# Performance work log

Hardware: AMD Instinct MI355X
Metric: run time of the kernel (lower is better)

The kernel has to match this reference:

```python
import jax, jax.numpy as jnp
from jax import lax
import numpy as np

CH = 16
STAGES = 6
DN = ('NDHWC', 'DHWIO', 'NDHWC')


def setup_inputs() -> dict:
    key = jax.random.key(0)
    ks = jax.random.split(key, 16)
    B, G = 8, 64
    x = jax.random.normal(ks[0], (B, G, G, G, 1), dtype=jnp.float32)
    mask = jax.random.randint(ks[1], (B, G, G, G), 0, 2, dtype=jnp.int32)
    meta = jax.random.normal(ks[2], (B, 3), dtype=jnp.float32)
    sched = jax.random.normal(ks[3], (B, 128), dtype=jnp.float32)
    s = 0.05
    w_stem = jax.random.normal(ks[4], (5, 5, 5, 1, CH), dtype=jnp.float32) * s
    w_stages = jax.random.normal(ks[5], (STAGES, 3, 3, 3, CH, CH), dtype=jnp.float32) * s
    meta_w1 = jax.random.normal(ks[6], (3, 32), dtype=jnp.float32) * s
    meta_b1 = jnp.zeros((32,), jnp.float32)
    meta_w2 = jax.random.normal(ks[7], (32, 16), dtype=jnp.float32) * s
    meta_b2 = jnp.zeros((16,), jnp.float32)
    mat_w = jax.random.normal(ks[8], (CH * STAGES + 16, 128), dtype=jnp.float32) * s
    mat_b = jnp.zeros((128,), jnp.float32)
    sch_w = jax.random.normal(ks[9], (128, 128), dtype=jnp.float32) * s
    sch_b = jnp.zeros((128,), jnp.float32)
    f1_w = jax.random.normal(ks[10], (256, 128), dtype=jnp.float32) * s
    f1_b = jnp.zeros((128,), jnp.float32)
    f2_w = jax.random.normal(ks[11], (128, 1), dtype=jnp.float32) * s
    f2_b = jnp.zeros((1,), jnp.float32)
    return dict(x=x, mask=mask, meta=meta, sched=sched, w_stem=w_stem,
                w_stages=w_stages, meta_w1=meta_w1, meta_b1=meta_b1,
                meta_w2=meta_w2, meta_b2=meta_b2, mat_w=mat_w, mat_b=mat_b,
                sch_w=sch_w, sch_b=sch_b, f1_w=f1_w, f1_b=f1_b,
                f2_w=f2_w, f2_b=f2_b)


def _pool_mask(m):
    # ME stride-2 output coords = unique(coords // 2): 2x2x2 max-pool, ceil sizes
    return lax.reduce_window(m, jnp.float32(0), lax.max,
                             (1, 2, 2, 2), (1, 2, 2, 2), 'SAME')


def reference(x, mask, meta, sched, w_stem, w_stages, meta_w1, meta_b1,
              meta_w2, meta_b2, mat_w, mat_b, sch_w, sch_b,
              f1_w, f1_b, f2_w, f2_b):
    m = mask.astype(x.dtype)
    feats = x * m[..., None]                       # zero features off-mask
    y = lax.conv_general_dilated(feats, w_stem, (1, 1, 1), 'SAME',
                                 dimension_numbers=DN)
    y = jnp.maximum(y * m[..., None], 0.0)         # stem: conv + mask + ReLU
    pools = []
    for i in range(STAGES):
        y = lax.conv_general_dilated(y, w_stages[i], (2, 2, 2),
                                     [(1, 1), (1, 1), (1, 1)],
                                     dimension_numbers=DN)
        m = _pool_mask(m)
        y = jnp.maximum(y * m[..., None], 0.0)
        denom = jnp.maximum(m.sum(axis=(1, 2, 3)), 1.0)   # occupied voxels
        pools.append(y.sum(axis=(1, 2, 3)) / denom[:, None])
    pools = jnp.concatenate(pools, axis=1)                 # [B, CH*STAGES]
    h = jax.nn.relu(meta[:, :3] @ meta_w1 + meta_b1)
    meta_emb = h @ meta_w2 + meta_b2                        # [B,16]
    m_emb = jax.nn.relu(jnp.concatenate([pools, meta_emb], 1) @ mat_w + mat_b)
    s_emb = jax.nn.relu(sched @ sch_w + sch_b)
    z = jnp.concatenate([m_emb, s_emb], axis=1)             # [B,256]
    z = jax.nn.relu(z @ f1_w + f1_b)
    return z @ f2_w + f2_b                                  # [B,1]
```

## Files before the change

### kernel.cpp

```cpp
#include <hip/hip_runtime.h>

#define CH 16
#define NB 8

typedef unsigned short u16;
typedef unsigned int u32;
typedef __attribute__((ext_vector_type(8))) short s16x8;
typedef __attribute__((ext_vector_type(4))) float f32x4;

__device__ __forceinline__ float bflo(u32 u) { return __uint_as_float(u << 16); }
__device__ __forceinline__ float bfhi(u32 u) { return __uint_as_float(u & 0xffff0000u); }
__device__ __forceinline__ u32 bfrnd(float f) {
  u32 u = __float_as_uint(f);
  return (u + 0x7fffu + ((u >> 16) & 1u)) >> 16;
}
__device__ __forceinline__ u32 packbf(float lo, float hi) {
  return bfrnd(lo) | (bfrnd(hi) << 16);
}

__global__ __launch_bounds__(256) void bprep_kernel(
    const float* __restrict__ w_stg, u16* __restrict__ bpre)
{
  const int e = blockIdx.x * 256 + (int)threadIdx.x;
  if (e >= 3 * 7168) return;
  const int s = e / 7168, r0 = e % 7168;
  const int i = r0 >> 9;
  const int r = r0 & 511;
  const int l = r >> 3, j = r & 7;
  const int tap = 2 * i + (l >> 5);
  const int cin = ((l >> 4) & 1) * 8 + j;
  const int n = l & 15;
  const float* w = w_stg + s * 27 * 256;
  const float val = (tap < 27) ? w[(tap * 16 + cin) * 16 + n] : 0.f;
  bpre[s * 7168 + i * 512 + l * 8 + j] = (u16)bfrnd(val);
}

__global__ __launch_bounds__(256) void stem_mfma(
    const float* __restrict__ x, const int* __restrict__ mask,
    const float* __restrict__ wst, u16* __restrict__ yout,
    float* __restrict__ pool_sum, float* __restrict__ cnt)
{
  __shared__ u16 tl[144 * 24];
  __shared__ u16 cp[8 * 1168];

  const int b = blockIdx.y;
  const int u = blockIdx.x;
  const int tb = ((u & 7) << 6) | (u >> 3);
  const int z0 = (tb >> 6) * 8;
  const int y0 = ((tb >> 3) & 7) * 8;
  const int x0 = (tb & 7) * 8;
  const int tid = threadIdx.x;

  if (tb == 0) {
    if (tid < 96) pool_sum[b * 96 + tid] = 0.f;
    else if (tid < 102) cnt[b * 6 + (tid - 96)] = 0.f;
  }

  const int lane = tid & 63;
  const int wv = tid >> 6;
  const int n = lane & 15;
  const int quad = lane >> 4;
  const int vy = n >> 2, vx = n & 3;

  s16x8 wf[7];
#pragma unroll
  for (int i = 0; i < 7; ++i) {
    const int r = i * 4 + quad;
#pragma unroll
    for (int j = 0; j < 8; ++j) {
      float v = 0.f;
      if (r < 25 && j < 5) v = wst[(r * 5 + j) * 16 + n];
      wf[i][j] = (short)bfrnd(v);
    }
  }

  for (int i = tid; i < 1728; i += 256) {
    const int row = i / 12;
    const int lx = i - row * 12;
    const int lz = row / 12;
    const int ly = row - lz * 12;
    const int gz = z0 + lz - 2, gy = y0 + ly - 2, gx = x0 + lx - 2;
    float v = 0.f;
    if ((unsigned)gz < 64u && (unsigned)gy < 64u && (unsigned)gx < 64u) {
      const int gi = ((b * 64 + gz) * 64 + gy) * 64 + gx;
      v = x[gi] * (float)mask[gi];
    }
    tl[row * 24 + lx] = (u16)bfrnd(v);
  }
  __syncthreads();

  if (tid < 144) {
    const uint4 a = *(const uint4*)&tl[tid * 24];
    const uint2 bq = *(const uint2*)&tl[tid * 24 + 8];
    u32 c[7];
    c[0] = a.x; c[1] = a.y; c[2] = a.z; c[3] = a.w;
    c[4] = bq.x; c[5] = bq.y; c[6] = 0u;
    u32 d[7];
#pragma unroll
    for (int k = 0; k < 6; ++k) d[k] = (c[k] >> 16) | (c[k + 1] << 16);
    d[6] = c[6] >> 16;
    uint4* dst = (uint4*)&cp[tid * 8];
    dst[0 * 146] = make_uint4(c[0], c[1], c[2], c[3]);
    dst[1 * 146] = make_uint4(d[0], d[1], d[2], d[3]);
    dst[2 * 146] = make_uint4(c[1], c[2], c[3], c[4]);
    dst[3 * 146] = make_uint4(d[1], d[2], d[3], d[4]);
    dst[4 * 146] = make_uint4(c[2], c[3], c[4], c[5]);
    dst[5 * 146] = make_uint4(d[2], d[3], d[4], d[5]);
    dst[6 * 146] = make_uint4(c[3], c[4], c[5], c[6]);
    dst[7 * 146] = make_uint4(d[3], d[4], d[5], d[6]);
  }
  __syncthreads();

  int doff[7];
#pragma unroll
  for (int i = 0; i < 7; ++i) {
    const int r = i * 4 + quad;
    doff[i] = (r < 25) ? ((r / 5) * 12 + (r % 5)) * 8 : 0;
  }

  for (int s = 0; s < 8; ++s) {
    const int sz = (s >> 2) * 4, sy = ((s >> 1) & 1) * 4, sx = (s & 1) * 4;
    const int base =
        (sx + vx) * 1168 + (((sz + wv) * 12) + (sy + vy)) * 8;
    f32x4 acc = {0.f, 0.f, 0.f, 0.f};
#pragma unroll
    for (int i = 0; i < 7; ++i) {
      const s16x8 bf = *(const s16x8*)&cp[base + doff[i]];
      acc = __builtin_amdgcn_mfma_f32_16x16x32_bf16(wf[i], bf, acc, 0, 0, 0);
    }
    const int Z = z0 + sz + wv, Y = y0 + sy + vy, X = x0 + sx + vx;
    const int gi = ((b * 64 + Z) * 64 + Y) * 64 + X;
    const float mv = (float)mask[gi];
    const float f0 = fmaxf(acc[0], 0.f) * mv;
    const float f1 = fmaxf(acc[1], 0.f) * mv;
    const float f2 = fmaxf(acc[2], 0.f) * mv;
    const float f3 = fmaxf(acc[3], 0.f) * mv;
    uint2* op = (uint2*)(yout + (size_t)gi * CH + quad * 4);
    op[0] = make_uint2(packbf(f0, f1), packbf(f2, f3));
  }
}

__global__ __launch_bounds__(256) void stage_mfma4(
    const u16* __restrict__ yin, const u16* __restrict__ bpre,
    const int* __restrict__ m_in_i, const float* __restrict__ m_in_f,
    u16* __restrict__ yout, float* __restrict__ m_out,
    float* __restrict__ pool_sum, float* __restrict__ cnt,
    const int S, const int stage)
{
  __shared__ u16 lb[14 * 512];
  __shared__ float lC[4 * 16 * 17];
  __shared__ float lmp[256];

  const int So = S >> 1;
  const int nvox = So * So * So;
  const int b = blockIdx.y;
  const int tid = threadIdx.x;
  const int vg0 = blockIdx.x * 256;

  {
    const uint4* src = (const uint4*)bpre;
    uint4* dst = (uint4*)lb;
    for (int e = tid; e < 896; e += 256) dst[e] = src[e];
  }

  {
    const int vox = vg0 + tid;
    const int oz = vox / (So * So);
    const int oy = (vox / So) % So;
    const int ox = vox % So;
    float mp = 0.f;
#pragma unroll
    for (int dz = 0; dz < 2; ++dz)
#pragma unroll
      for (int dy = 0; dy < 2; ++dy)
#pragma unroll
        for (int dx = 0; dx < 2; ++dx) {
          const int mi =
              ((b * S + 2 * oz + dz) * S + 2 * oy + dy) * S + 2 * ox + dx;
          const float mv = m_in_i ? (float)m_in_i[mi] : m_in_f[mi];
          mp = fmaxf(mp, mv);
        }
    lmp[tid] = mp;
  }
  __syncthreads();

  const int wv = tid >> 6;
  const int lane = tid & 63;
  const int m = lane & 15;
  const int quad = lane >> 4;
  const int qh = quad >> 1;
  const int qlo = quad & 1;

  int izb[4], iyb[4], ixb[4];
#pragma unroll
  for (int g = 0; g < 4; ++g) {
    const int vox = vg0 + wv * 64 + g * 16 + m;
    const int oz = vox / (So * So);
    const int oy = (vox / So) % So;
    const int ox = vox % So;
    izb[g] = 2 * oz - 1;
    iyb[g] = 2 * oy - 1;
    ixb[g] = 2 * ox - 1;
  }

  const s16x8* lbv = (const s16x8*)lb;
  f32x4 acc[4];
#pragma unroll
  for (int g = 0; g < 4; ++g) acc[g] = (f32x4){0.f, 0.f, 0.f, 0.f};

#pragma unroll
  for (int i = 0; i < 14; ++i) {
    const int t0 = 2 * i, t1 = 2 * i + 1;
    const int dz0 = t0 / 9, dy0 = (t0 / 3) % 3, dx0 = t0 % 3;
    const int dz1 = (t1 < 27) ? t1 / 9 : 1;
    const int dy1 = (t1 < 27) ? (t1 / 3) % 3 : 1;
    const int dx1 = (t1 < 27) ? t1 % 3 : 1;
    const int dzq = qh ? dz1 : dz0;
    const int dyq = qh ? dy1 : dy0;
    const int dxq = qh ? dx1 : dx0;

    uint4 ar[4];
#pragma unroll
    for (int g = 0; g < 4; ++g) {
      const int iz = izb[g] + dzq;
      const int iy = iyb[g] + dyq;
      const int ix = ixb[g] + dxq;
      const bool valid = (unsigned)iz < (unsigned)S &&
                         (unsigned)iy < (unsigned)S &&
                         (unsigned)ix < (unsigned)S;
      const int izc = min(max(iz, 0), S - 1);
      const int iyc = min(max(iy, 0), S - 1);
      const int ixc = min(max(ix, 0), S - 1);
      const size_t addr =
          (size_t)(((b * S + izc) * S + iyc) * S + ixc) * 16 + qlo * 8;
      uint4 v = *(const uint4*)(yin + addr);
      v.x = valid ? v.x : 0u;
      v.y = valid ? v.y : 0u;
      v.z = valid ? v.z : 0u;
      v.w = valid ? v.w : 0u;
      ar[g] = v;
    }
    const s16x8 bfrag = lbv[i * 64 + lane];
#pragma unroll
    for (int g = 0; g < 4; ++g)
      acc[g] = __builtin_amdgcn_mfma_f32_16x16x32_bf16(
          __builtin_bit_cast(s16x8, ar[g]), bfrag, acc[g], 0, 0, 0);
  }

  float psum = 0.f;
#pragma unroll
  for (int g = 0; g < 4; ++g) {
    __syncthreads();
    {
      float* lCw = lC + wv * 272;
      const int n = lane & 15;
#pragma unroll
      for (int reg = 0; reg < 4; ++reg) {
        const int row = quad * 4 + reg;
        lCw[row * 17 + n] =
            fmaxf(acc[g][reg], 0.f) * lmp[wv * 64 + g * 16 + row];
      }
    }
    __syncthreads();
    {
      const int vox_l = tid >> 2;
      const int cg = (tid & 3) * 4;
      const float* src = lC + (vox_l >> 4) * 272 + (vox_l & 15) * 17 + cg;
      const float f0 = src[0], f1 = src[1], f2 = src[2], f3 = src[3];
      const int lv = (vox_l >> 4) * 64 + g * 16 + (vox_l & 15);
      const size_t gi = (size_t)b * nvox + vg0 + lv;
      uint2* op = (uint2*)(yout + gi * 16 + cg);
      op[0] = make_uint2(packbf(f0, f1), packbf(f2, f3));
      if ((tid & 3) == 0) m_out[gi] = lmp[lv];
    }
    if (tid < 16) {
      float s = 0.f;
#pragma unroll 16
      for (int v = 0; v < 64; ++v)
        s += lC[(v >> 4) * 272 + (v & 15) * 17 + tid];
      psum += s;
    }
  }
  if (tid < 16) {
    atomicAdd(&pool_sum[(b * 6 + stage) * 16 + tid], psum);
  } else if (tid == 16) {
    float c = 0.f;
#pragma unroll 16
    for (int v = 0; v < 256; ++v) c += lmp[v];
    atomicAdd(&cnt[b * 6 + stage], c);
  }
}

__global__ __launch_bounds__(256) void tail_kernel(
    const u16* __restrict__ y3g, const float* __restrict__ m3g,
    const float* __restrict__ wstg,
    const float* __restrict__ meta, const float* __restrict__ sched,
    const float* __restrict__ mw1, const float* __restrict__ mb1,
    const float* __restrict__ mw2, const float* __restrict__ mb2,
    const float* __restrict__ matw, const float* __restrict__ matb,
    const float* __restrict__ schw, const float* __restrict__ schb,
    const float* __restrict__ f1w, const float* __restrict__ f1b,
    const float* __restrict__ f2w, const float* __restrict__ f2b,
    const float* __restrict__ pool_sum, const float* __restrict__ cnt,
    float* __restrict__ out)
{
  const int b = blockIdx.x;
  const int t = threadIdx.x;
  __shared__ float ly3[8 * 8 * 8 * 16];
  __shared__ float lm3[512];
  __shared__ float ly4[4 * 4 * 4 * 16];
  __shared__ float lm4[64];
  __shared__ float ly5[8 * 16];
  __shared__ float lm5[8];
  __shared__ float lsum[3][16];
  __shared__ float lcnt[3];
  __shared__ float invec[112];
  __shared__ float hbuf[32];
  __shared__ float zbuf[256];
  __shared__ float part[2];

  const uint4* yb = (const uint4*)(y3g + (size_t)b * 8192);
  for (int i = t; i < 1024; i += 256) {
    const uint4 p = yb[i];
    float* d = &ly3[i * 8];
    d[0] = bflo(p.x); d[1] = bfhi(p.x);
    d[2] = bflo(p.y); d[3] = bfhi(p.y);
    d[4] = bflo(p.z); d[5] = bfhi(p.z);
    d[6] = bflo(p.w); d[7] = bfhi(p.w);
  }
  for (int i = t; i < 512; i += 256) lm3[i] = m3g[b * 512 + i];
  __syncthreads();

  {
    const float* w = wstg + 3 * 27 * 256;
    const int vox = t >> 2, cog = (t & 3) * 4;
    const int oz = vox >> 4, oy = (vox >> 2) & 3, ox = vox & 3;
    float acc[4] = {0.f, 0.f, 0.f, 0.f};
#pragma unroll
    for (int dz = 0; dz < 3; ++dz)
#pragma unroll
      for (int dy = 0; dy < 3; ++dy)
#pragma unroll
        for (int dx = 0; dx < 3; ++dx) {
          const int iz = 2 * oz + dz - 1, iy = 2 * oy + dy - 1,
                    ix = 2 * ox + dx - 1;
          const float s = ((unsigned)iz < 8u && (unsigned)iy < 8u &&
                           (unsigned)ix < 8u) ? 1.f : 0.f;
          const int idx = ((min(max(iz, 0), 7) * 8 + min(max(iy, 0), 7)) * 8 +
                           min(max(ix, 0), 7)) * 16;
          const float* wp = w + ((dz * 3 + dy) * 3 + dx) * 256;
#pragma unroll
          for (int ci = 0; ci < 16; ++ci) {
            const float v = ly3[idx + ci] * s;
#pragma unroll
            for (int c = 0; c < 4; ++c)
              acc[c] = fmaf(v, wp[ci * 16 + cog + c], acc[c]);
          }
        }
    float mp = 0.f;
#pragma unroll
    for (int dz = 0; dz < 2; ++dz)
#pragma unroll
      for (int dy = 0; dy < 2; ++dy)
#pragma unroll
        for (int dx = 0; dx < 2; ++dx)
          mp = fmaxf(mp, lm3[((2 * oz + dz) * 8 + 2 * oy + dy) * 8 +
                             2 * ox + dx]);
#pragma unroll
    for (int c = 0; c < 4; ++c)
      ly4[vox * 16 + cog + c] = fmaxf(acc[c], 0.f) * mp;
    if (cog == 0) lm4[vox] = mp;
  }
  __syncthreads();

  if (t < 16) {
    float s = 0.f;
#pragma unroll 16
    for (int v = 0; v < 64; ++v) s += ly4[v * 16 + t];
    lsum[0][t] = s;
  } else if (t == 16) {
    float s = 0.f;
#pragma unroll 16
    for (int v = 0; v < 64; ++v) s += lm4[v];
    lcnt[0] = s;
  }
  float s4val = 0.f, s4mp = 0.f;
  const int vox4 = (t >> 4) & 7, co4 = t & 15;
  if (t < 128) {
    const float* w = wstg + 4 * 27 * 256;
    const int oz = vox4 >> 2, oy = (vox4 >> 1) & 1, ox = vox4 & 1;
    float acc = 0.f;
#pragma unroll
    for (int dz = 0; dz < 3; ++dz)
#pragma unroll
      for (int dy = 0; dy < 3; ++dy)
#pragma unroll
        for (int dx = 0; dx < 3; ++dx) {
          const int iz = 2 * oz + dz - 1, iy = 2 * oy + dy - 1,
                    ix = 2 * ox + dx - 1;
          const float s = ((unsigned)iz < 4u && (unsigned)iy < 4u &&
                           (unsigned)ix < 4u) ? 1.f : 0.f;
          const int idx = ((min(max(iz, 0), 3) * 4 + min(max(iy, 0), 3)) * 4 +
                           min(max(ix, 0), 3)) * 16;
          const float* wp = w + ((dz * 3 + dy) * 3 + dx) * 256 + co4;
#pragma unroll
          for (int ci = 0; ci < 16; ++ci)
            acc = fmaf(ly4[idx + ci] * s, wp[ci * 16], acc);
        }
    float mp = 0.f;
#pragma unroll
    for (int dz = 0; dz < 2; ++dz)
#pragma unroll
      for (int dy = 0; dy < 2; ++dy)
#pragma unroll
        for (int dx = 0; dx < 2; ++dx)
          mp = fmaxf(mp, lm4[((2 * (vox4 >> 2) + dz) * 4 +
                              2 * ((vox4 >> 1) & 1) + dy) * 4 +
                             2 * (vox4 & 1) + dx]);
    s4val = fmaxf(acc, 0.f) * mp;
    s4mp = mp;
  }
  __syncthreads();
  if (t < 128) {
    ly5[vox4 * 16 + co4] = s4val;
    if (co4 == 0) lm5[vox4] = s4mp;
  }
  __syncthreads();

  if (t < 16) {
    float s = 0.f;
#pragma unroll
    for (int v = 0; v < 8; ++v) s += ly5[v * 16 + t];
    lsum[1][t] = s;
  } else if (t == 16) {
    lcnt[1] = lm5[0] + lm5[1] + lm5[2] + lm5[3] + lm5[4] + lm5[5] + lm5[6] +
              lm5[7];
  }
  if (t >= 64 && t < 80) {
    const int co = t - 64;
    const float* w = wstg + 5 * 27 * 256;
    float acc = 0.f;
#pragma unroll
    for (int dz = 0; dz < 3; ++dz)
#pragma unroll
      for (int dy = 0; dy < 3; ++dy)
#pragma unroll
        for (int dx = 0; dx < 3; ++dx) {
          const int iz = dz - 1, iy = dy - 1, ix = dx - 1;
          const float s = ((unsigned)iz < 2u && (unsigned)iy < 2u &&
                           (unsigned)ix < 2u) ? 1.f : 0.f;
          const int idx = ((min(max(iz, 0), 1) * 2 + min(max(iy, 0), 1)) * 2 +
                           min(max(ix, 0), 1)) * 16;
          const float* wp = w + ((dz * 3 + dy) * 3 + dx) * 256 + co;
#pragma unroll
          for (int ci = 0; ci < 16; ++ci)
            acc = fmaf(ly5[idx + ci] * s, wp[ci * 16], acc);
        }
    float mp = 0.f;
#pragma unroll
    for (int v = 0; v < 8; ++v) mp = fmaxf(mp, lm5[v]);
    lsum[2][co] = fmaxf(acc, 0.f) * mp;
    if (co == 0) lcnt[2] = mp;
  }
  __syncthreads();

  if (t < 48) {
    const int s = t >> 4;
    invec[t] = pool_sum[b * 96 + t] / fmaxf(cnt[b * 6 + s], 1.f);
  } else if (t < 96) {
    const int s = (t >> 4) - 3;
    invec[t] = lsum[s][t & 15] / fmaxf(lcnt[s], 1.f);
  } else if (t < 128) {
    const int j = t - 96;
    float h = mb1[j];
#pragma unroll
    for (int k = 0; k < 3; ++k) h = fmaf(meta[b * 3 + k], mw1[k * 32 + j], h);
    hbuf[j] = fmaxf(h, 0.f);
  }
  __syncthreads();
  if (t < 16) {
    float e = mb2[t];
#pragma unroll
    for (int j = 0; j < 32; ++j) e = fmaf(hbuf[j], mw2[j * 16 + t], e);
    invec[96 + t] = e;
  }
  __syncthreads();
  if (t < 128) {
    float a = matb[t];
#pragma unroll 16
    for (int k = 0; k < 112; ++k) a = fmaf(invec[k], matw[k * 128 + t], a);
    zbuf[t] = fmaxf(a, 0.f);
    float s = schb[t];
#pragma unroll 16
    for (int k = 0; k < 128; ++k)
      s = fmaf(sched[b * 128 + k], schw[k * 128 + t], s);
    zbuf[128 + t] = fmaxf(s, 0.f);
  }
  __syncthreads();
  if (t < 128) {
    float a = f1b[t];
#pragma unroll 16
    for (int k = 0; k < 256; ++k) a = fmaf(zbuf[k], f1w[k * 128 + t], a);
    float v = fmaxf(a, 0.f) * f2w[t];
#pragma unroll
    for (int off = 32; off > 0; off >>= 1) v += __shfl_xor(v, off, 64);
    if ((t & 63) == 0) part[t >> 6] = v;
  }
  __syncthreads();
  if (t == 0) out[b] = part[0] + part[1] + f2b[0];
}

extern "C" void kernel_launch(void* const* d_in, const int* in_sizes, int n_in,
                              void* d_out, int out_size, void* d_ws,
                              size_t ws_size, hipStream_t stream)
{
  (void)in_sizes; (void)n_in; (void)out_size; (void)ws_size;
  const float* x      = (const float*)d_in[0];
  const int*   mask   = (const int*)  d_in[1];
  const float* meta   = (const float*)d_in[2];
  const float* sched  = (const float*)d_in[3];
  const float* w_stem = (const float*)d_in[4];
  const float* w_stg  = (const float*)d_in[5];
  const float* mw1    = (const float*)d_in[6];
  const float* mb1    = (const float*)d_in[7];
  const float* mw2    = (const float*)d_in[8];
  const float* mb2    = (const float*)d_in[9];
  const float* matw   = (const float*)d_in[10];
  const float* matb   = (const float*)d_in[11];
  const float* schw   = (const float*)d_in[12];
  const float* schb   = (const float*)d_in[13];
  const float* f1w    = (const float*)d_in[14];
  const float* f1b    = (const float*)d_in[15];
  const float* f2w    = (const float*)d_in[16];
  const float* f2b    = (const float*)d_in[17];
  float* out = (float*)d_out;

  char* ws = (char*)d_ws;
  size_t off = 0;
  auto alloc = [&](size_t nbytes) -> void* {
    void* p = ws + off;
    off += (nbytes + 255) & ~(size_t)255;
    return p;
  };

  u16* y0 = (u16*)alloc((size_t)NB * 64 * 64 * 64 * CH * 2);
  u16* y1 = (u16*)alloc((size_t)NB * 32 * 32 * 32 * CH * 2);
  u16* y2 = (u16*)alloc((size_t)NB * 16 * 16 * 16 * CH * 2);
  u16* y3 = (u16*)alloc((size_t)NB * 8 * 8 * 8 * CH * 2);
  float* m1 = (float*)alloc((size_t)NB * 32 * 32 * 32 * 4);
  float* m2 = (float*)alloc((size_t)NB * 16 * 16 * 16 * 4);
  float* m3 = (float*)alloc((size_t)NB * 8 * 8 * 8 * 4);
  float* pool_sum = (float*)alloc((NB * 96 + NB * 6) * 4);
  float* cnt = pool_sum + NB * 96;
  u16* bpre = (u16*)alloc(3 * 7168 * 2);

  bprep_kernel<<<84, 256, 0, stream>>>(w_stg, bpre);

  stem_mfma<<<dim3(512, NB), 256, 0, stream>>>(x, mask, w_stem, y0,
                                               pool_sum, cnt);

  stage_mfma4<<<dim3(128, NB), 256, 0, stream>>>(
      y0, bpre + 0 * 7168, mask, (const float*)nullptr, y1, m1,
      pool_sum, cnt, 64, 0);
  stage_mfma4<<<dim3(16, NB), 256, 0, stream>>>(
      y1, bpre + 1 * 7168, (const int*)nullptr, m1, y2, m2,
      pool_sum, cnt, 32, 1);
  stage_mfma4<<<dim3(2, NB), 256, 0, stream>>>(
      y2, bpre + 2 * 7168, (const int*)nullptr, m2, y3, m3,
      pool_sum, cnt, 16, 2);

  tail_kernel<<<NB, 256, 0, stream>>>(y3, m3, w_stg, meta, sched,
                                      mw1, mb1, mw2, mb2, matw, matb,
                                      schw, schb, f1w, f1b, f2w, f2b,
                                      pool_sum, cnt, out);
}
```

Baseline: 227.3 us.

## Use MFMA for tail stage-3 conv and split tail work across all threads

The tail kernel's stage-3 conv now runs on bf16 MFMA. It uses a fourth slab of prepacked weights produced by the extended bprep kernel, and each wave reduces a share of the taps before a shared-memory partial-sum reduction. The stage 4/5 convs and the f1 and schedule layers are split across more threads, with the partial sums combined afterwards. The meta MLP is moved earlier to overlap with other work. The intent is to shorten the serial tail, which runs on only 8 blocks. In exchange it adds extra syncs and shared memory, and the stage-3 conv now runs in bf16.

```diff
diff --git a/kernel.cpp b/kernel.cpp
--- a/kernel.cpp
+++ b/kernel.cpp
@@ -22,7 +22,7 @@
     const float* __restrict__ w_stg, u16* __restrict__ bpre)
 {
   const int e = blockIdx.x * 256 + (int)threadIdx.x;
-  if (e >= 3 * 7168) return;
+  if (e >= 4 * 7168) return;
   const int s = e / 7168, r0 = e % 7168;
   const int i = r0 >> 9;
   const int r = r0 & 511;
@@ -293,6 +293,7 @@
 
 __global__ __launch_bounds__(256) void tail_kernel(
     const u16* __restrict__ y3g, const float* __restrict__ m3g,
+    const u16* __restrict__ bpre,
     const float* __restrict__ wstg,
     const float* __restrict__ meta, const float* __restrict__ sched,
     const float* __restrict__ mw1, const float* __restrict__ mb1,
@@ -306,57 +307,99 @@
 {
   const int b = blockIdx.x;
   const int t = threadIdx.x;
-  __shared__ float ly3[8 * 8 * 8 * 16];
+  __shared__ u16 ty3[8192];
   __shared__ float lm3[512];
-  __shared__ float ly4[4 * 4 * 4 * 16];
+  __shared__ float pb[4 * 64 * 17];
+  __shared__ float ly4[64 * 16];
   __shared__ float lm4[64];
+  __shared__ float ps4[256];
   __shared__ float ly5[8 * 16];
   __shared__ float lm5[8];
+  __shared__ float ps5[128];
   __shared__ float lsum[3][16];
   __shared__ float lcnt[3];
   __shared__ float invec[112];
   __shared__ float hbuf[32];
   __shared__ float zbuf[256];
+  __shared__ float psf[256];
   __shared__ float part[2];
 
-  const uint4* yb = (const uint4*)(y3g + (size_t)b * 8192);
-  for (int i = t; i < 1024; i += 256) {
-    const uint4 p = yb[i];
-    float* d = &ly3[i * 8];
-    d[0] = bflo(p.x); d[1] = bfhi(p.x);
-    d[2] = bflo(p.y); d[3] = bfhi(p.y);
-    d[4] = bflo(p.z); d[5] = bfhi(p.z);
-    d[6] = bflo(p.w); d[7] = bfhi(p.w);
-  }
-  for (int i = t; i < 512; i += 256) lm3[i] = m3g[b * 512 + i];
-  __syncthreads();
-
   {
-    const float* w = wstg + 3 * 27 * 256;
-    const int vox = t >> 2, cog = (t & 3) * 4;
+    const uint4* yb = (const uint4*)(y3g + (size_t)b * 8192);
+    uint4* dst = (uint4*)ty3;
+    for (int i = t; i < 1024; i += 256) dst[i] = yb[i];
+    for (int i = t; i < 512; i += 256) lm3[i] = m3g[b * 512 + i];
+  }
+  __syncthreads();
+
+  {
+    const int lane = t & 63;
+    const int wv = t >> 6;
+    const int mm = lane & 15;
+    const int quad = lane >> 4;
+    const int qh = quad >> 1, qlo = quad & 1;
+
+    int iz0[4], iy0[4], ix0[4];
+#pragma unroll
+    for (int g = 0; g < 4; ++g) {
+      const int vox = g * 16 + mm;
+      iz0[g] = 2 * (vox >> 4) - 1;
+      iy0[g] = 2 * ((vox >> 2) & 3) - 1;
+      ix0[g] = 2 * (vox & 3) - 1;
+    }
+    f32x4 a3[4];
+#pragma unroll
+    for (int g = 0; g < 4; ++g) a3[g] = (f32x4){0.f, 0.f, 0.f, 0.f};
+    const s16x8* bp3 = (const s16x8*)(bpre + 3 * 7168);
+#pragma unroll
+    for (int ii = 0; ii < 4; ++ii) {
+      const int i = wv * 4 + ii;
+      if (i < 14) {
+        const int t0 = 2 * i, t1 = 2 * i + 1;
+        const int dz0 = t0 / 9, dy0 = (t0 / 3) % 3, dx0 = t0 % 3;
+        const int dz1 = (t1 < 27) ? t1 / 9 : 1;
+        const int dy1 = (t1 < 27) ? (t1 / 3) % 3 : 1;
+        const int dx1 = (t1 < 27) ? t1 % 3 : 1;
+        const int dzq = qh ? dz1 : dz0;
+        const int dyq = qh ? dy1 : dy0;
+        const int dxq = qh ? dx1 : dx0;
+        uint4 ar[4];
+#pragma unroll
+        for (int g = 0; g < 4; ++g) {
+          const int iz = iz0[g] + dzq;
+          const int iy = iy0[g] + dyq;
+          const int ix = ix0[g] + dxq;
+          const bool valid = (unsigned)iz < 8u && (unsigned)iy < 8u &&
+                             (unsigned)ix < 8u;
+          const int izc = min(max(iz, 0), 7);
+          const int iyc = min(max(iy, 0), 7);
+          const int ixc = min(max(ix, 0), 7);
+          const int ad = ((izc * 8 + iyc) * 8 + ixc) * 16 + qlo * 8;
+          uint4 v = *(const uint4*)&ty3[ad];
+          v.x = valid ? v.x : 0u;
+          v.y = valid ? v.y : 0u;
+          v.z = valid ? v.z : 0u;
+          v.w = valid ? v.w : 0u;
+          ar[g] = v;
+        }
+        const s16x8 bf = bp3[i * 64 + lane];
+#pragma unroll
+        for (int g = 0; g < 4; ++g)
+          a3[g] = __builtin_amdgcn_mfma_f32_16x16x32_bf16(
+              __builtin_bit_cast(s16x8, ar[g]), bf, a3[g], 0, 0, 0);
+      }
+    }
+#pragma unroll
+    for (int g = 0; g < 4; ++g)
+#pragma unroll
+      for (int reg = 0; reg < 4; ++reg)
+        pb[wv * 1088 + (g * 16 + quad * 4 + reg) * 17 + mm] = a3[g][reg];
+  }
+  __syncthreads();
+
+  {
+    const int vox = t >> 2, cg = (t & 3) * 4;
     const int oz = vox >> 4, oy = (vox >> 2) & 3, ox = vox & 3;
-    float acc[4] = {0.f, 0.f, 0.f, 0.f};
-#pragma unroll
-    for (int dz = 0; dz < 3; ++dz)
-#pragma unroll
-      for (int dy = 0; dy < 3; ++dy)
-#pragma unroll
-        for (int dx = 0; dx < 3; ++dx) {
-          const int iz = 2 * oz + dz - 1, iy = 2 * oy + dy - 1,
-                    ix = 2 * ox + dx - 1;
-          const float s = ((unsigned)iz < 8u && (unsigned)iy < 8u &&
-                           (unsigned)ix < 8u) ? 1.f : 0.f;
-          const int idx = ((min(max(iz, 0), 7) * 8 + min(max(iy, 0), 7)) * 8 +
-                           min(max(ix, 0), 7)) * 16;
-          const float* wp = w + ((dz * 3 + dy) * 3 + dx) * 256;
-#pragma unroll
-          for (int ci = 0; ci < 16; ++ci) {
-            const float v = ly3[idx + ci] * s;
-#pragma unroll
-            for (int c = 0; c < 4; ++c)
-              acc[c] = fmaf(v, wp[ci * 16 + cog + c], acc[c]);
-          }
-        }
     float mp = 0.f;
 #pragma unroll
     for (int dz = 0; dz < 2; ++dz)
@@ -367,9 +410,13 @@
           mp = fmaxf(mp, lm3[((2 * oz + dz) * 8 + 2 * oy + dy) * 8 +
                              2 * ox + dx]);
 #pragma unroll
-    for (int c = 0; c < 4; ++c)
-      ly4[vox * 16 + cog + c] = fmaxf(acc[c], 0.f) * mp;
-    if (cog == 0) lm4[vox] = mp;
+    for (int c = 0; c < 4; ++c) {
+      const int ch = cg + c;
+      const float s = pb[vox * 17 + ch] + pb[1088 + vox * 17 + ch] +
+                      pb[2176 + vox * 17 + ch] + pb[3264 + vox * 17 + ch];
+      ly4[vox * 16 + ch] = fmaxf(s, 0.f) * mp;
+    }
+    if (cg == 0) lm4[vox] = mp;
   }
   __syncthreads();
 
@@ -384,29 +431,35 @@
     for (int v = 0; v < 64; ++v) s += lm4[v];
     lcnt[0] = s;
   }
-  float s4val = 0.f, s4mp = 0.f;
-  const int vox4 = (t >> 4) & 7, co4 = t & 15;
-  if (t < 128) {
+  {
     const float* w = wstg + 4 * 27 * 256;
+    const int o = t >> 1, kh = t & 1;
+    const int vox4 = o >> 4, co = o & 15;
     const int oz = vox4 >> 2, oy = (vox4 >> 1) & 1, ox = vox4 & 1;
     float acc = 0.f;
 #pragma unroll
-    for (int dz = 0; dz < 3; ++dz)
-#pragma unroll
-      for (int dy = 0; dy < 3; ++dy)
-#pragma unroll
-        for (int dx = 0; dx < 3; ++dx) {
-          const int iz = 2 * oz + dz - 1, iy = 2 * oy + dy - 1,
-                    ix = 2 * ox + dx - 1;
-          const float s = ((unsigned)iz < 4u && (unsigned)iy < 4u &&
-                           (unsigned)ix < 4u) ? 1.f : 0.f;
-          const int idx = ((min(max(iz, 0), 3) * 4 + min(max(iy, 0), 3)) * 4 +
-                           min(max(ix, 0), 3)) * 16;
-          const float* wp = w + ((dz * 3 + dy) * 3 + dx) * 256 + co4;
-#pragma unroll
-          for (int ci = 0; ci < 16; ++ci)
-            acc = fmaf(ly4[idx + ci] * s, wp[ci * 16], acc);
-        }
+    for (int tt = 0; tt < 14; ++tt) {
+      const int tap = tt + (kh ? 14 : 0);
+      if (tap < 27) {
+        const int dz = tap / 9, dy = (tap / 3) % 3, dx = tap % 3;
+        const int iz = 2 * oz + dz - 1, iy = 2 * oy + dy - 1,
+                  ix = 2 * ox + dx - 1;
+        const float s = ((unsigned)iz < 4u && (unsigned)iy < 4u &&
+                         (unsigned)ix < 4u) ? 1.f : 0.f;
+        const int idx = ((min(max(iz, 0), 3) * 4 + min(max(iy, 0), 3)) * 4 +
+                         min(max(ix, 0), 3)) * 16;
+        const float* wp = w + tap * 256 + co;
+#pragma unroll
+        for (int ci = 0; ci < 16; ++ci)
+          acc = fmaf(ly4[idx + ci] * s, wp[ci * 16], acc);
+      }
+    }
+    ps4[t] = acc;
+  }
+  __syncthreads();
+
+  if (t < 128) {
+    const int vox4 = t >> 4, co = t & 15;
     float mp = 0.f;
 #pragma unroll
     for (int dz = 0; dz < 2; ++dz)
@@ -417,13 +470,8 @@
           mp = fmaxf(mp, lm4[((2 * (vox4 >> 2) + dz) * 4 +
                               2 * ((vox4 >> 1) & 1) + dy) * 4 +
                              2 * (vox4 & 1) + dx]);
-    s4val = fmaxf(acc, 0.f) * mp;
-    s4mp = mp;
-  }
-  __syncthreads();
-  if (t < 128) {
-    ly5[vox4 * 16 + co4] = s4val;
-    if (co4 == 0) lm5[vox4] = s4mp;
+    ly5[t] = fmaxf(ps4[2 * t] + ps4[2 * t + 1], 0.f) * mp;
+    if (co == 0) lm5[vox4] = mp;
   }
   __syncthreads();
 
@@ -436,31 +484,44 @@
     lcnt[1] = lm5[0] + lm5[1] + lm5[2] + lm5[3] + lm5[4] + lm5[5] + lm5[6] +
               lm5[7];
   }
-  if (t >= 64 && t < 80) {
-    const int co = t - 64;
+  if (t < 128) {
     const float* w = wstg + 5 * 27 * 256;
+    const int co = t & 15, k8 = t >> 4;
     float acc = 0.f;
 #pragma unroll
-    for (int dz = 0; dz < 3; ++dz)
-#pragma unroll
-      for (int dy = 0; dy < 3; ++dy)
-#pragma unroll
-        for (int dx = 0; dx < 3; ++dx) {
-          const int iz = dz - 1, iy = dy - 1, ix = dx - 1;
-          const float s = ((unsigned)iz < 2u && (unsigned)iy < 2u &&
-                           (unsigned)ix < 2u) ? 1.f : 0.f;
-          const int idx = ((min(max(iz, 0), 1) * 2 + min(max(iy, 0), 1)) * 2 +
-                           min(max(ix, 0), 1)) * 16;
-          const float* wp = w + ((dz * 3 + dy) * 3 + dx) * 256 + co;
-#pragma unroll
-          for (int ci = 0; ci < 16; ++ci)
-            acc = fmaf(ly5[idx + ci] * s, wp[ci * 16], acc);
-        }
+    for (int tt = 0; tt < 4; ++tt) {
+      const int tap = k8 * 4 + tt;
+      if (tap < 27) {
+        const int dz = tap / 9, dy = (tap / 3) % 3, dx = tap % 3;
+        const int iz = dz - 1, iy = dy - 1, ix = dx - 1;
+        const float s = ((unsigned)iz < 2u && (unsigned)iy < 2u &&
+                         (unsigned)ix < 2u) ? 1.f : 0.f;
+        const int idx = ((min(max(iz, 0), 1) * 2 + min(max(iy, 0), 1)) * 2 +
+                         min(max(ix, 0), 1)) * 16;
+        const float* wp = w + tap * 256 + co;
+#pragma unroll
+        for (int ci = 0; ci < 16; ++ci)
+          acc = fmaf(ly5[idx + ci] * s, wp[ci * 16], acc);
+      }
+    }
+    ps5[t] = acc;
+  }
+  __syncthreads();
+
+  if (t < 16) {
+    float s = ps5[t] + ps5[16 + t] + ps5[32 + t] + ps5[48 + t] +
+              ps5[64 + t] + ps5[80 + t] + ps5[96 + t] + ps5[112 + t];
     float mp = 0.f;
 #pragma unroll
     for (int v = 0; v < 8; ++v) mp = fmaxf(mp, lm5[v]);
-    lsum[2][co] = fmaxf(acc, 0.f) * mp;
-    if (co == 0) lcnt[2] = mp;
+    lsum[2][t] = fmaxf(s, 0.f) * mp;
+    if (t == 0) lcnt[2] = mp;
+  } else if (t >= 96 && t < 128) {
+    const int j = t - 96;
+    float h = mb1[j];
+#pragma unroll
+    for (int k = 0; k < 3; ++k) h = fmaf(meta[b * 3 + k], mw1[k * 32 + j], h);
+    hbuf[j] = fmaxf(h, 0.f);
   }
   __syncthreads();
 
@@ -470,37 +531,44 @@
   } else if (t < 96) {
     const int s = (t >> 4) - 3;
     invec[t] = lsum[s][t & 15] / fmaxf(lcnt[s], 1.f);
-  } else if (t < 128) {
+  } else if (t < 112) {
     const int j = t - 96;
-    float h = mb1[j];
-#pragma unroll
-    for (int k = 0; k < 3; ++k) h = fmaf(meta[b * 3 + k], mw1[k * 32 + j], h);
-    hbuf[j] = fmaxf(h, 0.f);
-  }
-  __syncthreads();
-  if (t < 16) {
-    float e = mb2[t];
-#pragma unroll
-    for (int j = 0; j < 32; ++j) e = fmaf(hbuf[j], mw2[j * 16 + t], e);
-    invec[96 + t] = e;
-  }
-  __syncthreads();
+    float e = mb2[j];
+#pragma unroll
+    for (int k = 0; k < 32; ++k) e = fmaf(hbuf[k], mw2[k * 16 + j], e);
+    invec[t] = e;
+  }
+  __syncthreads();
+
   if (t < 128) {
     float a = matb[t];
 #pragma unroll 16
     for (int k = 0; k < 112; ++k) a = fmaf(invec[k], matw[k * 128 + t], a);
     zbuf[t] = fmaxf(a, 0.f);
-    float s = schb[t];
+  } else {
+    const int c = t - 128;
+    float s = schb[c];
 #pragma unroll 16
     for (int k = 0; k < 128; ++k)
-      s = fmaf(sched[b * 128 + k], schw[k * 128 + t], s);
-    zbuf[128 + t] = fmaxf(s, 0.f);
-  }
-  __syncthreads();
+      s = fmaf(sched[b * 128 + k], schw[k * 128 + c], s);
+    zbuf[128 + c] = fmaxf(s, 0.f);
+  }
+  __syncthreads();
+
+  {
+    const int col = t & 127, kh = t >> 7;
+    float a = 0.f;
+#pragma unroll 16
+    for (int kk = 0; kk < 128; ++kk) {
+      const int k = kh * 128 + kk;
+      a = fmaf(zbuf[k], f1w[k * 128 + col], a);
+    }
+    psf[t] = a;
+  }
+  __syncthreads();
+
   if (t < 128) {
-    float a = f1b[t];
-#pragma unroll 16
-    for (int k = 0; k < 256; ++k) a = fmaf(zbuf[k], f1w[k * 128 + t], a);
+    const float a = psf[t] + psf[128 + t] + f1b[t];
     float v = fmaxf(a, 0.f) * f2w[t];
 #pragma unroll
     for (int off = 32; off > 0; off >>= 1) v += __shfl_xor(v, off, 64);
@@ -552,9 +620,9 @@
   float* m3 = (float*)alloc((size_t)NB * 8 * 8 * 8 * 4);
   float* pool_sum = (float*)alloc((NB * 96 + NB * 6) * 4);
   float* cnt = pool_sum + NB * 96;
-  u16* bpre = (u16*)alloc(3 * 7168 * 2);
-
-  bprep_kernel<<<84, 256, 0, stream>>>(w_stg, bpre);
+  u16* bpre = (u16*)alloc(4 * 7168 * 2);
+
+  bprep_kernel<<<112, 256, 0, stream>>>(w_stg, bpre);
 
   stem_mfma<<<dim3(512, NB), 256, 0, stream>>>(x, mask, w_stem, y0,
                                                pool_sum, cnt);
@@ -569,7 +637,7 @@
       y2, bpre + 2 * 7168, (const int*)nullptr, m2, y3, m3,
       pool_sum, cnt, 16, 2);
 
-  tail_kernel<<<NB, 256, 0, stream>>>(y3, m3, w_stg, meta, sched,
+  tail_kernel<<<NB, 256, 0, stream>>>(y3, m3, bpre, w_stg, meta, sched,
                                       mw1, mb1, mw2, mb2, matw, matb,
                                       schw, schb, f1w, f1b, f2w, f2b,
                                       pool_sum, cnt, out);
```

After: 212.8 us. 6.4% less time.
